# Performance work log

Measured on AMD Instinct MI355X. Metric: run time of the kernel, lower is better.

Reference implementation:

```python
import jax, jax.numpy as jnp
import numpy as np

N_NODES = 50000
N_EDGES = 800000
D_FEAT = 64
EDGE_DIM = 64


def setup_inputs() -> dict:
    key = jax.random.key(0)
    k1, k2, k3, k4 = jax.random.split(key, 4)
    node_feats = jax.random.normal(k1, (N_NODES, D_FEAT), dtype=jnp.float32)
    senders = jax.random.randint(k2, (N_EDGES,), 0, N_NODES, dtype=jnp.int32)
    receivers = jax.random.randint(k3, (N_EDGES,), 0, N_NODES, dtype=jnp.int32)
    # Dense(edge_dim) applied to concat([recv, send]) of width 2*D_FEAT
    W = jax.random.normal(k4, (2 * D_FEAT, EDGE_DIM), dtype=jnp.float32) / np.sqrt(2.0 * D_FEAT)
    b = jnp.zeros((EDGE_DIM,), dtype=jnp.float32)
    return {"node_feats": node_feats, "senders": senders, "receivers": receivers, "W": W, "b": b}


def reference(node_feats, senders, receivers, W, b):
    # gather node features at each edge endpoint: [E, D]
    feats_send = node_feats[senders]
    feats_recv = node_feats[receivers]
    # concat(recv, send) -> [E, 2D], Dense + tanh -> [E, edge_dim]
    edge_feats = jnp.concatenate([feats_recv, feats_send], axis=-1)
    return jnp.tanh(edge_feats @ W + b)
```

## Files before the change

### kernel.cpp

```cpp
#include <hip/hip_runtime.h>

#define N_EDGES 800000
#define N_NODES 50000
#define D 64

typedef __attribute__((ext_vector_type(8))) short bf16x8;
typedef __attribute__((ext_vector_type(4))) float f32x4;

#if __has_builtin(__builtin_amdgcn_exp2f)
#define EXP2F(x) __builtin_amdgcn_exp2f(x)
#else
#define EXP2F(x) __expf(0.69314718055994531f * (x))
#endif

__device__ __forceinline__ unsigned short f2bf(float f) {
    unsigned int u = __float_as_uint(f);
    u += 0x7fffu + ((u >> 16) & 1u);
    return (unsigned short)(u >> 16);
}
__device__ __forceinline__ unsigned int pack2(float a, float b) {
    return (unsigned int)f2bf(a) | ((unsigned int)f2bf(b) << 16);
}

__global__ __launch_bounds__(256) void node_proj(
    const float* __restrict__ nf, const float* __restrict__ W,
    float* __restrict__ Pr, float* __restrict__ Ps)
{
    __shared__ bf16x8 lds_b[1024];

#pragma unroll
    for (int i = 0; i < 4; ++i) {
        const int idx = i * 256 + threadIdx.x;
        const int ki = idx >> 8;
        const int nt = (idx >> 6) & 3;
        const int l  = idx & 63;
        const int mm = l & 15, qq = l >> 4;
        const int kbase = ki * 32 + qq * 8;
        const int n = nt * 16 + mm;
        union { bf16x8 v; unsigned short h[8]; } cv;
#pragma unroll
        for (int j = 0; j < 8; ++j)
            cv.h[j] = f2bf(W[(kbase + j) * D + n]);
        lds_b[idx] = cv.v;
    }
    __syncthreads();

    const int lane = threadIdx.x & 63;
    const int m    = lane & 15;
    const int q    = lane >> 4;
    const int wid  = blockIdx.x * 4 + (threadIdx.x >> 6);
    const int n0   = wid * 64;

    bf16x8 a[2][4];
#pragma unroll
    for (int mt = 0; mt < 4; ++mt) {
        const int row = n0 + mt * 16 + m;
        const int rl  = row < N_NODES ? row : N_NODES - 1;
        const float* rp = nf + (long)rl * D;
#pragma unroll
        for (int kk = 0; kk < 2; ++kk) {
            const float4 lo = *(const float4*)(rp + kk * 32 + q * 8);
            const float4 hi = *(const float4*)(rp + kk * 32 + q * 8 + 4);
            union { bf16x8 v; unsigned int u[4]; } cv;
            cv.u[0] = pack2(lo.x, lo.y);
            cv.u[1] = pack2(lo.z, lo.w);
            cv.u[2] = pack2(hi.x, hi.y);
            cv.u[3] = pack2(hi.z, hi.w);
            a[kk][mt] = cv.v;
        }
    }

#pragma unroll
    for (int tab = 0; tab < 2; ++tab) {
        f32x4 acc[4][4];
#pragma unroll
        for (int mt = 0; mt < 4; ++mt)
#pragma unroll
            for (int nt = 0; nt < 4; ++nt)
                acc[mt][nt] = (f32x4)0.0f;

#pragma unroll
        for (int ki2 = 0; ki2 < 2; ++ki2) {
#pragma unroll
            for (int nt = 0; nt < 4; ++nt) {
                const bf16x8 bf = lds_b[((tab * 2 + ki2) * 4 + nt) * 64 + lane];
#pragma unroll
                for (int mt = 0; mt < 4; ++mt)
                    acc[mt][nt] = __builtin_amdgcn_mfma_f32_16x16x32_bf16(
                        bf, a[ki2][mt], acc[mt][nt], 0, 0, 0);
            }
        }

        float* __restrict__ P = tab ? Ps : Pr;
#pragma unroll
        for (int mt = 0; mt < 4; ++mt) {
            const int row = n0 + mt * 16 + m;
            if (row < N_NODES) {
                float* op = P + (long)row * D + q * 4;
#pragma unroll
                for (int nt = 0; nt < 4; ++nt)
                    *(f32x4*)(op + nt * 16) = acc[mt][nt];
            }
        }
    }
}

__global__ __launch_bounds__(256) void edge_act(
    const float* __restrict__ Pr, const float* __restrict__ Ps,
    const int*   __restrict__ senders, const int* __restrict__ receivers,
    const float* __restrict__ bias, float* __restrict__ out)
{
    const int t = blockIdx.x * 256 + threadIdx.x;
    const int e = t >> 2;
    const int c = t & 3;

    const int r = receivers[e];
    const int s = senders[e];
    const float* pr = Pr + (long)r * D + c * 4;
    const float* ps = Ps + (long)s * D + c * 4;
    float*       op = out + (long)e * D + c * 4;

    f32x4 pa[4], pb[4], bb[4];
#pragma unroll
    for (int s4 = 0; s4 < 4; ++s4) {
        pa[s4] = *(const f32x4*)(pr + s4 * 16);
        pb[s4] = *(const f32x4*)(ps + s4 * 16);
        bb[s4] = *(const f32x4*)(bias + s4 * 16 + c * 4);
    }

    const float C2L = 2.8853900817779268f;
#pragma unroll
    for (int s4 = 0; s4 < 4; ++s4) {
        const f32x4 x = pa[s4] + pb[s4];
        f32x4 y;
#pragma unroll
        for (int k = 0; k < 4; ++k) {
            const float tt = EXP2F(__builtin_fmaf(x[k], C2L, bb[s4][k] * C2L));
            const float rc = __builtin_amdgcn_rcpf(tt + 1.0f);
            y[k] = __builtin_fmaf(-2.0f, rc, 1.0f);
        }
        __builtin_nontemporal_store(y, (f32x4*)(op + s4 * 16));
    }
}

extern "C" void kernel_launch(void* const* d_in, const int* in_sizes, int n_in,
                              void* d_out, int out_size, void* d_ws, size_t ws_size,
                              hipStream_t stream) {
    const float* node_feats = (const float*)d_in[0];
    const int*   senders    = (const int*)d_in[1];
    const int*   receivers  = (const int*)d_in[2];
    const float* W          = (const float*)d_in[3];
    const float* bias       = (const float*)d_in[4];
    float*       out        = (float*)d_out;

    float* Pr = (float*)d_ws;
    float* Ps = Pr + (size_t)N_NODES * D;

    const int np_blocks = (N_NODES + 255) / 256;
    node_proj<<<np_blocks, 256, 0, stream>>>(node_feats, W, Pr, Ps);

    const int ea_blocks = (N_EDGES * 4) / 256;
    edge_act<<<ea_blocks, 256, 0, stream>>>(Pr, Ps, senders, receivers, bias, out);
}
```

Measured before the change: 276.1 us.

## Store node projections in fp16, fold bias, split tables across blocks

Node projection tables are now stored as fp16 instead of fp32, which halves the gathered bytes per edge in the edge kernel. The bias add moves into the node projection for the receiver table, so the edge kernel no longer loads bias. The edge kernel now gives each thread 16 contiguous features instead of strided chunks. The node projection grid is doubled so each block computes a single table, giving more parallelism. fp16 storage adds rounding error to the pre-activation values.

```diff
diff --git a/kernel.cpp b/kernel.cpp
--- a/kernel.cpp
+++ b/kernel.cpp
@@ -3,9 +3,12 @@
 #define N_EDGES 800000
 #define N_NODES 50000
 #define D 64
+#define NPB 196
 
-typedef __attribute__((ext_vector_type(8))) short bf16x8;
-typedef __attribute__((ext_vector_type(4))) float f32x4;
+typedef __attribute__((ext_vector_type(8))) short    bf16x8;
+typedef __attribute__((ext_vector_type(4))) float    f32x4;
+typedef __attribute__((ext_vector_type(8))) _Float16 f16x8;
+typedef __attribute__((ext_vector_type(4))) _Float16 f16x4;
 
 #if __has_builtin(__builtin_amdgcn_exp2f)
 #define EXP2F(x) __builtin_amdgcn_exp2f(x)
@@ -24,18 +27,22 @@
 
 __global__ __launch_bounds__(256) void node_proj(
     const float* __restrict__ nf, const float* __restrict__ W,
-    float* __restrict__ Pr, float* __restrict__ Ps)
+    const float* __restrict__ bias,
+    _Float16* __restrict__ Pr, _Float16* __restrict__ Ps)
 {
-    __shared__ bf16x8 lds_b[1024];
+    __shared__ bf16x8 lds_b[512];
+
+    const int tab = blockIdx.x >= NPB;
+    const int bid = tab ? blockIdx.x - NPB : blockIdx.x;
 
 #pragma unroll
-    for (int i = 0; i < 4; ++i) {
+    for (int i = 0; i < 2; ++i) {
         const int idx = i * 256 + threadIdx.x;
-        const int ki = idx >> 8;
-        const int nt = (idx >> 6) & 3;
-        const int l  = idx & 63;
-        const int mm = l & 15, qq = l >> 4;
-        const int kbase = ki * 32 + qq * 8;
+        const int ki2 = idx >> 8;
+        const int nt  = (idx >> 6) & 3;
+        const int l   = idx & 63;
+        const int mm  = l & 15, qq = l >> 4;
+        const int kbase = (tab * 2 + ki2) * 32 + qq * 8;
         const int n = nt * 16 + mm;
         union { bf16x8 v; unsigned short h[8]; } cv;
 #pragma unroll
@@ -48,7 +55,7 @@
     const int lane = threadIdx.x & 63;
     const int m    = lane & 15;
     const int q    = lane >> 4;
-    const int wid  = blockIdx.x * 4 + (threadIdx.x >> 6);
+    const int wid  = bid * 4 + (threadIdx.x >> 6);
     const int n0   = wid * 64;
 
     bf16x8 a[2][4];
@@ -70,45 +77,53 @@
         }
     }
 
+    f32x4 acc[4][4];
 #pragma unroll
-    for (int tab = 0; tab < 2; ++tab) {
-        f32x4 acc[4][4];
+    for (int mt = 0; mt < 4; ++mt)
 #pragma unroll
-        for (int mt = 0; mt < 4; ++mt)
-#pragma unroll
-            for (int nt = 0; nt < 4; ++nt)
-                acc[mt][nt] = (f32x4)0.0f;
+        for (int nt = 0; nt < 4; ++nt)
+            acc[mt][nt] = (f32x4)0.0f;
 
 #pragma unroll
-        for (int ki2 = 0; ki2 < 2; ++ki2) {
+    for (int ki2 = 0; ki2 < 2; ++ki2) {
+#pragma unroll
+        for (int nt = 0; nt < 4; ++nt) {
+            const bf16x8 bf = lds_b[(ki2 * 4 + nt) * 64 + lane];
+#pragma unroll
+            for (int mt = 0; mt < 4; ++mt)
+                acc[mt][nt] = __builtin_amdgcn_mfma_f32_16x16x32_bf16(
+                    bf, a[ki2][mt], acc[mt][nt], 0, 0, 0);
+        }
+    }
+
+    f32x4 bv[4];
+#pragma unroll
+    for (int nt = 0; nt < 4; ++nt) {
+        const float4 b4 = *(const float4*)(bias + nt * 16 + q * 4);
+        bv[nt] = tab ? (f32x4)0.0f : (f32x4){b4.x, b4.y, b4.z, b4.w};
+    }
+
+    _Float16* __restrict__ P = tab ? Ps : Pr;
+#pragma unroll
+    for (int mt = 0; mt < 4; ++mt) {
+        const int row = n0 + mt * 16 + m;
+        if (row < N_NODES) {
+            _Float16* op = P + (long)row * D + q * 4;
 #pragma unroll
             for (int nt = 0; nt < 4; ++nt) {
-                const bf16x8 bf = lds_b[((tab * 2 + ki2) * 4 + nt) * 64 + lane];
-#pragma unroll
-                for (int mt = 0; mt < 4; ++mt)
-                    acc[mt][nt] = __builtin_amdgcn_mfma_f32_16x16x32_bf16(
-                        bf, a[ki2][mt], acc[mt][nt], 0, 0, 0);
-            }
-        }
-
-        float* __restrict__ P = tab ? Ps : Pr;
-#pragma unroll
-        for (int mt = 0; mt < 4; ++mt) {
-            const int row = n0 + mt * 16 + m;
-            if (row < N_NODES) {
-                float* op = P + (long)row * D + q * 4;
-#pragma unroll
-                for (int nt = 0; nt < 4; ++nt)
-                    *(f32x4*)(op + nt * 16) = acc[mt][nt];
+                const f32x4 v = acc[mt][nt] + bv[nt];
+                const f16x4 h = {(_Float16)v[0], (_Float16)v[1],
+                                 (_Float16)v[2], (_Float16)v[3]};
+                *(f16x4*)(op + nt * 16) = h;
             }
         }
     }
 }
 
 __global__ __launch_bounds__(256) void edge_act(
-    const float* __restrict__ Pr, const float* __restrict__ Ps,
+    const _Float16* __restrict__ Pr, const _Float16* __restrict__ Ps,
     const int*   __restrict__ senders, const int* __restrict__ receivers,
-    const float* __restrict__ bias, float* __restrict__ out)
+    float* __restrict__ out)
 {
     const int t = blockIdx.x * 256 + threadIdx.x;
     const int e = t >> 2;
@@ -116,30 +131,29 @@
 
     const int r = receivers[e];
     const int s = senders[e];
-    const float* pr = Pr + (long)r * D + c * 4;
-    const float* ps = Ps + (long)s * D + c * 4;
-    float*       op = out + (long)e * D + c * 4;
+    const _Float16* pr = Pr + r * D + c * 16;
+    const _Float16* ps = Ps + s * D + c * 16;
+    float*          op = out + (long)e * D + c * 16;
 
-    f32x4 pa[4], pb[4], bb[4];
-#pragma unroll
-    for (int s4 = 0; s4 < 4; ++s4) {
-        pa[s4] = *(const f32x4*)(pr + s4 * 16);
-        pb[s4] = *(const f32x4*)(ps + s4 * 16);
-        bb[s4] = *(const f32x4*)(bias + s4 * 16 + c * 4);
-    }
+    const f16x8 a0 = *(const f16x8*)(pr);
+    const f16x8 a1 = *(const f16x8*)(pr + 8);
+    const f16x8 b0 = *(const f16x8*)(ps);
+    const f16x8 b1 = *(const f16x8*)(ps + 8);
 
     const float C2L = 2.8853900817779268f;
 #pragma unroll
-    for (int s4 = 0; s4 < 4; ++s4) {
-        const f32x4 x = pa[s4] + pb[s4];
+    for (int g = 0; g < 4; ++g) {
         f32x4 y;
 #pragma unroll
         for (int k = 0; k < 4; ++k) {
-            const float tt = EXP2F(__builtin_fmaf(x[k], C2L, bb[s4][k] * C2L));
+            const int j = g * 4 + k;
+            const float x = (j < 8) ? (float)a0[j] + (float)b0[j]
+                                    : (float)a1[j - 8] + (float)b1[j - 8];
+            const float tt = EXP2F(x * C2L);
             const float rc = __builtin_amdgcn_rcpf(tt + 1.0f);
             y[k] = __builtin_fmaf(-2.0f, rc, 1.0f);
         }
-        __builtin_nontemporal_store(y, (f32x4*)(op + s4 * 16));
+        __builtin_nontemporal_store(y, (f32x4*)(op + g * 4));
     }
 }
 
@@ -153,12 +167,11 @@
     const float* bias       = (const float*)d_in[4];
     float*       out        = (float*)d_out;
 
-    float* Pr = (float*)d_ws;
-    float* Ps = Pr + (size_t)N_NODES * D;
+    _Float16* Pr = (_Float16*)d_ws;
+    _Float16* Ps = Pr + (size_t)N_NODES * D;
 
-    const int np_blocks = (N_NODES + 255) / 256;
-    node_proj<<<np_blocks, 256, 0, stream>>>(node_feats, W, Pr, Ps);
+    node_proj<<<2 * NPB, 256, 0, stream>>>(node_feats, W, bias, Pr, Ps);
 
     const int ea_blocks = (N_EDGES * 4) / 256;
-    edge_act<<<ea_blocks, 256, 0, stream>>>(Pr, Ps, senders, receivers, bias, out);
+    edge_act<<<ea_blocks, 256, 0, stream>>>(Pr, Ps, senders, receivers, out);
 }
```

New measurement: 311.6 us. 12.8% more time.
